# Kernel tuning notes

Hardware: AMD Instinct MI355X
Metric: run time of the kernel (lower is better)

Reference implementation:

```python
import jax, jax.numpy as jnp
import numpy as np

B, N, H, E = 4, 256, 128, 32

def setup_inputs() -> dict:
    key = jax.random.key(0)
    ks = jax.random.split(key, 7)
    s = 0.05
    return {
        "node_h": jax.random.normal(ks[0], (B, N, H), dtype=jnp.float32),
        "dart_h": jax.random.normal(ks[1], (B, N, N, H), dtype=jnp.float32),
        "edge_x": jax.random.normal(ks[2], (B, N, N, E), dtype=jnp.float32),
        "W1": jax.random.normal(ks[3], (3 * H + E, H), dtype=jnp.float32) * s,
        "b1": jnp.zeros((H,), dtype=jnp.float32),
        "W2": jax.random.normal(ks[4], (H, H), dtype=jnp.float32) * s,
        "b2": jnp.zeros((H,), dtype=jnp.float32),
    }

def reference(node_h, dart_h, edge_x, W1, b1, W2, b2):
    # Split first-layer weight by concat blocks [src | dst | dart_h | edge_x]
    W1s, W1d, W1h, W1e = W1[:H], W1[H:2*H], W1[2*H:3*H], W1[3*H:]
    # Equivalent to mlp(cat([src_expand, dst_expand, dart_h, edge_x])) but
    # computes the small [B,N,H] matmuls before broadcasting to [B,N,N,H].
    pre = (jnp.einsum('bih,hk->bik', node_h, W1s)[:, :, None, :]
           + jnp.einsum('bjh,hk->bjk', node_h, W1d)[:, None, :, :]
           + jnp.einsum('bijh,hk->bijk', dart_h, W1h)
           + jnp.einsum('bije,ek->bijk', edge_x, W1e)
           + b1)
    h = jax.nn.relu(pre)
    return jnp.einsum('bijh,hk->bijk', h, W2) + b2
```

## Files before the change

kernel.cpp:

```cpp
#include <hip/hip_runtime.h>
#include <hip/hip_bf16.h>


typedef __attribute__((ext_vector_type(8))) short bf16x8;
typedef __attribute__((ext_vector_type(4))) short bf16x4;
typedef __attribute__((ext_vector_type(4))) float f32x4;

__device__ __forceinline__ unsigned short f2bf(float f) {
  union { float f; unsigned u; } v; v.f = f;
  unsigned r = v.u + 0x7FFFu + ((v.u >> 16) & 1u);
  return (unsigned short)(r >> 16);
}

__global__ void prep_kernel(const float* __restrict__ node, const float* __restrict__ W1,
                            const float* __restrict__ b1, const float* __restrict__ W2,
                            float* __restrict__ S, float* __restrict__ DT,
                            unsigned short* __restrict__ W1hT, unsigned short* __restrict__ W1eT,
                            unsigned short* __restrict__ W2T) {
  const int t = threadIdx.x;
  if (blockIdx.x < 64) {
    __shared__ float nrow[16 * 128];
    const int bi0 = blockIdx.x * 16;
    const float4* src = reinterpret_cast<const float4*>(node + bi0 * 128);
    float4* dst = reinterpret_cast<float4*>(nrow);
    dst[t] = src[t];
    dst[t + 256] = src[t + 256];
    __syncthreads();
    const int kc = t & 127, half = t >> 7;
    float s[8], d[8];
#pragma unroll
    for (int r = 0; r < 8; ++r) { s[r] = 0.f; d[r] = 0.f; }
    for (int h = 0; h < 128; ++h) {
      float ws = W1[h * 128 + kc];
      float wd = W1[(128 + h) * 128 + kc];
#pragma unroll
      for (int r = 0; r < 8; ++r) {
        float nv = nrow[(half * 8 + r) * 128 + h];
        s[r] = fmaf(nv, ws, s[r]);
        d[r] = fmaf(nv, wd, d[r]);
      }
    }
    const float bv = b1[kc];
    const int b = bi0 >> 8, i0 = bi0 & 255;
#pragma unroll
    for (int r = 0; r < 8; ++r) {
      int row = half * 8 + r;
      S[(bi0 + row) * 128 + kc] = s[r] + bv;
      DT[(b * 128 + kc) * 256 + i0 + row] = d[r];
    }
  } else {
    int gid = (blockIdx.x - 64) * 256 + t;
    for (int idx = gid; idx < 16384; idx += 2048)
      W1hT[idx] = f2bf(W1[(256 + (idx & 127)) * 128 + (idx >> 7)]);
    for (int idx = gid; idx < 4096; idx += 2048)
      W1eT[idx] = f2bf(W1[(384 + (idx & 31)) * 128 + (idx >> 5)]);
    for (int idx = gid; idx < 16384; idx += 2048)
      W2T[idx] = f2bf(W2[(idx & 127) * 128 + (idx >> 7)]);
  }
}

#define LDD 136
#define LDE 40

__launch_bounds__(256, 2)
__global__ void fused_kernel(const float* __restrict__ dart, const float* __restrict__ edge,
                             const float* __restrict__ S, const float* __restrict__ DT,
                             const unsigned short* __restrict__ W1hT,
                             const unsigned short* __restrict__ W1eT,
                             const unsigned short* __restrict__ W2T,
                             const float* __restrict__ b2, float* __restrict__ out) {
  __shared__ unsigned short sDart[64 * LDD];
  __shared__ unsigned short sEdge[64 * LDE];
  __shared__ unsigned short sH[64 * LDD];

  const int tid = threadIdx.x;
  const int lane = tid & 63;
  const int w = tid >> 6;
  const int g = lane >> 4;
  const int lj = lane & 15;

  bf16x8 wh[2][4], w2f[4][2], we[2];
#pragma unroll
  for (int kt = 0; kt < 2; ++kt)
#pragma unroll
    for (int hs = 0; hs < 4; ++hs)
      wh[kt][hs] = *reinterpret_cast<const bf16x8*>(&W1hT[(w * 32 + kt * 16 + lj) * 128 + hs * 32 + g * 8]);
#pragma unroll
  for (int kt = 0; kt < 2; ++kt)
    we[kt] = *reinterpret_cast<const bf16x8*>(&W1eT[(w * 32 + kt * 16 + lj) * 32 + g * 8]);
#pragma unroll
  for (int ks = 0; ks < 4; ++ks)
#pragma unroll
    for (int nt = 0; nt < 2; ++nt)
      w2f[ks][nt] = *reinterpret_cast<const bf16x8*>(&W2T[(w * 32 + nt * 16 + lj) * 128 + ks * 32 + g * 8]);
  float b2v[2];
  b2v[0] = b2[w * 32 + lj];
  b2v[1] = b2[w * 32 + 16 + lj];

  for (int tile = blockIdx.x; tile < 4096; tile += gridDim.x) {
    const int m0 = tile * 64;
    const int bi = m0 >> 8;
    const int b = bi >> 8;
    const int j0 = m0 & 255;

    {
      const int row = tid >> 2, c0 = (tid & 3) * 32;
      const float4* src = reinterpret_cast<const float4*>(dart + (size_t)(m0 + row) * 128 + c0);
#pragma unroll
      for (int p = 0; p < 4; ++p) {
        float4 a = src[2 * p], c = src[2 * p + 1];
        bf16x8 pk;
        pk[0] = (short)f2bf(a.x); pk[1] = (short)f2bf(a.y);
        pk[2] = (short)f2bf(a.z); pk[3] = (short)f2bf(a.w);
        pk[4] = (short)f2bf(c.x); pk[5] = (short)f2bf(c.y);
        pk[6] = (short)f2bf(c.z); pk[7] = (short)f2bf(c.w);
        *reinterpret_cast<bf16x8*>(&sDart[row * LDD + c0 + p * 8]) = pk;
      }
      const int e0 = (tid & 3) * 8;
      const float4* esrc = reinterpret_cast<const float4*>(edge + (size_t)(m0 + row) * 32 + e0);
      float4 a = esrc[0], c = esrc[1];
      bf16x8 pk;
      pk[0] = (short)f2bf(a.x); pk[1] = (short)f2bf(a.y);
      pk[2] = (short)f2bf(a.z); pk[3] = (short)f2bf(a.w);
      pk[4] = (short)f2bf(c.x); pk[5] = (short)f2bf(c.y);
      pk[6] = (short)f2bf(c.z); pk[7] = (short)f2bf(c.w);
      *reinterpret_cast<bf16x8*>(&sEdge[row * LDE + e0]) = pk;
    }
    __syncthreads();

    f32x4 acc1[2][4];
#pragma unroll
    for (int kt = 0; kt < 2; ++kt)
#pragma unroll
      for (int jt = 0; jt < 4; ++jt) acc1[kt][jt] = (f32x4){0.f, 0.f, 0.f, 0.f};

#pragma unroll
    for (int hs = 0; hs < 4; ++hs) {
#pragma unroll
      for (int jt = 0; jt < 4; ++jt) {
        bf16x8 bd = *reinterpret_cast<const bf16x8*>(&sDart[(jt * 16 + lj) * LDD + hs * 32 + g * 8]);
        acc1[0][jt] = __builtin_amdgcn_mfma_f32_16x16x32_bf16(wh[0][hs], bd, acc1[0][jt], 0, 0, 0);
        acc1[1][jt] = __builtin_amdgcn_mfma_f32_16x16x32_bf16(wh[1][hs], bd, acc1[1][jt], 0, 0, 0);
      }
    }
#pragma unroll
    for (int jt = 0; jt < 4; ++jt) {
      bf16x8 be = *reinterpret_cast<const bf16x8*>(&sEdge[(jt * 16 + lj) * LDE + g * 8]);
      acc1[0][jt] = __builtin_amdgcn_mfma_f32_16x16x32_bf16(we[0], be, acc1[0][jt], 0, 0, 0);
      acc1[1][jt] = __builtin_amdgcn_mfma_f32_16x16x32_bf16(we[1], be, acc1[1][jt], 0, 0, 0);
    }

    {
      const float* Sp = S + bi * 128 + w * 32;
      const float* DTp = DT + ((b * 128 + w * 32) * 256) + j0;
#pragma unroll
      for (int kt = 0; kt < 2; ++kt) {
        float sv[4];
#pragma unroll
        for (int r = 0; r < 4; ++r) sv[r] = Sp[kt * 16 + g * 4 + r];
#pragma unroll
        for (int jt = 0; jt < 4; ++jt) {
          bf16x4 hp;
#pragma unroll
          for (int r = 0; r < 4; ++r) {
            int kc = kt * 16 + g * 4 + r;
            float dv = DTp[kc * 256 + jt * 16 + lj];
            float x = acc1[kt][jt][r] + sv[r] + dv;
            x = x > 0.f ? x : 0.f;
            hp[r] = (short)f2bf(x);
          }
          *reinterpret_cast<bf16x4*>(&sH[(jt * 16 + lj) * LDD + w * 32 + kt * 16 + g * 4]) = hp;
        }
      }
    }
    __syncthreads();

    f32x4 acc2[4][2];
#pragma unroll
    for (int jt = 0; jt < 4; ++jt)
#pragma unroll
      for (int nt = 0; nt < 2; ++nt) acc2[jt][nt] = (f32x4){0.f, 0.f, 0.f, 0.f};

#pragma unroll
    for (int ks = 0; ks < 4; ++ks) {
#pragma unroll
      for (int jt = 0; jt < 4; ++jt) {
        bf16x8 ah = *reinterpret_cast<const bf16x8*>(&sH[(jt * 16 + lj) * LDD + ks * 32 + g * 8]);
        acc2[jt][0] = __builtin_amdgcn_mfma_f32_16x16x32_bf16(ah, w2f[ks][0], acc2[jt][0], 0, 0, 0);
        acc2[jt][1] = __builtin_amdgcn_mfma_f32_16x16x32_bf16(ah, w2f[ks][1], acc2[jt][1], 0, 0, 0);
      }
    }

    float* op = out + (size_t)m0 * 128 + w * 32;
#pragma unroll
    for (int jt = 0; jt < 4; ++jt)
#pragma unroll
      for (int nt = 0; nt < 2; ++nt)
#pragma unroll
        for (int r = 0; r < 4; ++r)
          op[(size_t)(jt * 16 + g * 4 + r) * 128 + nt * 16 + lj] = acc2[jt][nt][r] + b2v[nt];
  }
}

extern "C" void kernel_launch(void* const* d_in, const int* in_sizes, int n_in,
                              void* d_out, int out_size, void* d_ws, size_t ws_size,
                              hipStream_t stream) {
  const float* node = (const float*)d_in[0];
  const float* dart = (const float*)d_in[1];
  const float* edge = (const float*)d_in[2];
  const float* W1   = (const float*)d_in[3];
  const float* b1   = (const float*)d_in[4];
  const float* W2   = (const float*)d_in[5];
  const float* b2   = (const float*)d_in[6];
  float* out = (float*)d_out;

  float* S  = (float*)d_ws;
  float* DT = S + 131072;
  unsigned short* W1hT = (unsigned short*)(DT + 131072);
  unsigned short* W1eT = W1hT + 16384;
  unsigned short* W2T  = W1eT + 4096;

  hipLaunchKernelGGL(prep_kernel, dim3(72), dim3(256), 0, stream,
                     node, W1, b1, W2, S, DT, W1hT, W1eT, W2T);
  hipLaunchKernelGGL(fused_kernel, dim3(4096), dim3(256), 0, stream,
                     dart, edge, S, DT, W1hT, W1eT, W2T, b2, out);
}
```

Measured before the change: 112.6 us.

## Process one full bi row per block with register prefetch of next tile

Each fused-kernel block now handles one (b,i) row of 256 j across four 64-row tiles. The next tile's dart and edge data are loaded into registers while the current tile's MFMAs run, which overlaps global-load latency with compute, and S and the weights are loaded once per block. The second GEMM swaps its operands so the output can be written as float4 rows, and the prep kernel uses more, smaller blocks for the S/DT precompute. In exchange the grid has fewer blocks and register pressure rises from the prefetch buffers.

```diff
diff --git a/kernel.cpp b/kernel.cpp
--- a/kernel.cpp
+++ b/kernel.cpp
@@ -18,38 +18,30 @@
                             unsigned short* __restrict__ W1hT, unsigned short* __restrict__ W1eT,
                             unsigned short* __restrict__ W2T) {
   const int t = threadIdx.x;
-  if (blockIdx.x < 64) {
-    __shared__ float nrow[16 * 128];
-    const int bi0 = blockIdx.x * 16;
-    const float4* src = reinterpret_cast<const float4*>(node + bi0 * 128);
-    float4* dst = reinterpret_cast<float4*>(nrow);
-    dst[t] = src[t];
-    dst[t + 256] = src[t + 256];
+  if (blockIdx.x < 256) {
+    __shared__ float nrow[4 * 128];
+    const int bi0 = blockIdx.x * 4;
+    if (t < 128)
+      reinterpret_cast<float4*>(nrow)[t] = reinterpret_cast<const float4*>(node + bi0 * 128)[t];
     __syncthreads();
     const int kc = t & 127, half = t >> 7;
-    float s[8], d[8];
-#pragma unroll
-    for (int r = 0; r < 8; ++r) { s[r] = 0.f; d[r] = 0.f; }
+    float s0 = 0.f, s1 = 0.f, d0 = 0.f, d1 = 0.f;
     for (int h = 0; h < 128; ++h) {
       float ws = W1[h * 128 + kc];
       float wd = W1[(128 + h) * 128 + kc];
-#pragma unroll
-      for (int r = 0; r < 8; ++r) {
-        float nv = nrow[(half * 8 + r) * 128 + h];
-        s[r] = fmaf(nv, ws, s[r]);
-        d[r] = fmaf(nv, wd, d[r]);
-      }
+      float n0 = nrow[(half * 2) * 128 + h];
+      float n1 = nrow[(half * 2 + 1) * 128 + h];
+      s0 = fmaf(n0, ws, s0); s1 = fmaf(n1, ws, s1);
+      d0 = fmaf(n0, wd, d0); d1 = fmaf(n1, wd, d1);
     }
     const float bv = b1[kc];
     const int b = bi0 >> 8, i0 = bi0 & 255;
-#pragma unroll
-    for (int r = 0; r < 8; ++r) {
-      int row = half * 8 + r;
-      S[(bi0 + row) * 128 + kc] = s[r] + bv;
-      DT[(b * 128 + kc) * 256 + i0 + row] = d[r];
-    }
+    S[(bi0 + half * 2) * 128 + kc] = s0 + bv;
+    S[(bi0 + half * 2 + 1) * 128 + kc] = s1 + bv;
+    DT[(b * 128 + kc) * 256 + i0 + half * 2] = d0;
+    DT[(b * 128 + kc) * 256 + i0 + half * 2 + 1] = d1;
   } else {
-    int gid = (blockIdx.x - 64) * 256 + t;
+    int gid = (blockIdx.x - 256) * 256 + t;
     for (int idx = gid; idx < 16384; idx += 2048)
       W1hT[idx] = f2bf(W1[(256 + (idx & 127)) * 128 + (idx >> 7)]);
     for (int idx = gid; idx < 4096; idx += 2048)
@@ -79,6 +71,10 @@
   const int g = lane >> 4;
   const int lj = lane & 15;
 
+  const int bi = blockIdx.x;
+  const int b = bi >> 8;
+  const size_t m_base = (size_t)bi * 256;
+
   bf16x8 wh[2][4], w2f[4][2], we[2];
 #pragma unroll
   for (int kt = 0; kt < 2; ++kt)
@@ -93,112 +89,165 @@
 #pragma unroll
     for (int nt = 0; nt < 2; ++nt)
       w2f[ks][nt] = *reinterpret_cast<const bf16x8*>(&W2T[(w * 32 + nt * 16 + lj) * 128 + ks * 32 + g * 8]);
-  float b2v[2];
-  b2v[0] = b2[w * 32 + lj];
-  b2v[1] = b2[w * 32 + 16 + lj];
-
-  for (int tile = blockIdx.x; tile < 4096; tile += gridDim.x) {
-    const int m0 = tile * 64;
-    const int bi = m0 >> 8;
-    const int b = bi >> 8;
-    const int j0 = m0 & 255;
-
+
+  float sv[2][4], b2v[2][4];
+#pragma unroll
+  for (int kt = 0; kt < 2; ++kt)
+#pragma unroll
+    for (int r = 0; r < 4; ++r)
+      sv[kt][r] = S[bi * 128 + w * 32 + kt * 16 + g * 4 + r];
+#pragma unroll
+  for (int nt = 0; nt < 2; ++nt)
+#pragma unroll
+    for (int r = 0; r < 4; ++r)
+      b2v[nt][r] = b2[w * 32 + nt * 16 + g * 4 + r];
+
+  const int srow = tid >> 2;
+  const int c0 = (tid & 3) * 32;
+  const int e0 = (tid & 3) * 8;
+
+  float4 rD[8], rE[2];
+
+  {
+    const float4* dsrc = reinterpret_cast<const float4*>(dart + (m_base + srow) * 128 + c0);
+#pragma unroll
+    for (int p = 0; p < 8; ++p) rD[p] = dsrc[p];
+    const float4* esrc = reinterpret_cast<const float4*>(edge + (m_base + srow) * 32 + e0);
+    rE[0] = esrc[0]; rE[1] = esrc[1];
+  }
+  {
+#pragma unroll
+    for (int p = 0; p < 4; ++p) {
+      float4 a = rD[2 * p], c = rD[2 * p + 1];
+      bf16x8 pk;
+      pk[0] = (short)f2bf(a.x); pk[1] = (short)f2bf(a.y);
+      pk[2] = (short)f2bf(a.z); pk[3] = (short)f2bf(a.w);
+      pk[4] = (short)f2bf(c.x); pk[5] = (short)f2bf(c.y);
+      pk[6] = (short)f2bf(c.z); pk[7] = (short)f2bf(c.w);
+      *reinterpret_cast<bf16x8*>(&sDart[srow * LDD + c0 + p * 8]) = pk;
+    }
+    float4 a = rE[0], c = rE[1];
+    bf16x8 pk;
+    pk[0] = (short)f2bf(a.x); pk[1] = (short)f2bf(a.y);
+    pk[2] = (short)f2bf(a.z); pk[3] = (short)f2bf(a.w);
+    pk[4] = (short)f2bf(c.x); pk[5] = (short)f2bf(c.y);
+    pk[6] = (short)f2bf(c.z); pk[7] = (short)f2bf(c.w);
+    *reinterpret_cast<bf16x8*>(&sEdge[srow * LDE + e0]) = pk;
+  }
+  __syncthreads();
+
+  for (int t = 0; t < 4; ++t) {
+    const int j0 = t * 64;
+
+    float dv[2][4][4];
     {
-      const int row = tid >> 2, c0 = (tid & 3) * 32;
-      const float4* src = reinterpret_cast<const float4*>(dart + (size_t)(m0 + row) * 128 + c0);
+      const float* DTp = DT + (size_t)(b * 128 + w * 32) * 256 + j0;
+#pragma unroll
+      for (int kt = 0; kt < 2; ++kt)
+#pragma unroll
+        for (int jt = 0; jt < 4; ++jt)
+#pragma unroll
+          for (int r = 0; r < 4; ++r)
+            dv[kt][jt][r] = DTp[(kt * 16 + g * 4 + r) * 256 + jt * 16 + lj];
+    }
+
+    if (t < 3) {
+      const float4* dsrc = reinterpret_cast<const float4*>(dart + (m_base + j0 + 64 + srow) * 128 + c0);
+#pragma unroll
+      for (int p = 0; p < 8; ++p) rD[p] = dsrc[p];
+      const float4* esrc = reinterpret_cast<const float4*>(edge + (m_base + j0 + 64 + srow) * 32 + e0);
+      rE[0] = esrc[0]; rE[1] = esrc[1];
+    }
+
+    f32x4 acc1[2][4];
+#pragma unroll
+    for (int kt = 0; kt < 2; ++kt)
+#pragma unroll
+      for (int jt = 0; jt < 4; ++jt) acc1[kt][jt] = (f32x4){0.f, 0.f, 0.f, 0.f};
+
+#pragma unroll
+    for (int hs = 0; hs < 4; ++hs) {
+#pragma unroll
+      for (int jt = 0; jt < 4; ++jt) {
+        bf16x8 bd = *reinterpret_cast<const bf16x8*>(&sDart[(jt * 16 + lj) * LDD + hs * 32 + g * 8]);
+        acc1[0][jt] = __builtin_amdgcn_mfma_f32_16x16x32_bf16(wh[0][hs], bd, acc1[0][jt], 0, 0, 0);
+        acc1[1][jt] = __builtin_amdgcn_mfma_f32_16x16x32_bf16(wh[1][hs], bd, acc1[1][jt], 0, 0, 0);
+      }
+    }
+#pragma unroll
+    for (int jt = 0; jt < 4; ++jt) {
+      bf16x8 be = *reinterpret_cast<const bf16x8*>(&sEdge[(jt * 16 + lj) * LDE + e0 - (tid & 3) * 8 + g * 8]);
+      acc1[0][jt] = __builtin_amdgcn_mfma_f32_16x16x32_bf16(we[0], be, acc1[0][jt], 0, 0, 0);
+      acc1[1][jt] = __builtin_amdgcn_mfma_f32_16x16x32_bf16(we[1], be, acc1[1][jt], 0, 0, 0);
+    }
+
+#pragma unroll
+    for (int kt = 0; kt < 2; ++kt) {
+#pragma unroll
+      for (int jt = 0; jt < 4; ++jt) {
+        bf16x4 hp;
+#pragma unroll
+        for (int r = 0; r < 4; ++r) {
+          float x = acc1[kt][jt][r] + sv[kt][r] + dv[kt][jt][r];
+          x = x > 0.f ? x : 0.f;
+          hp[r] = (short)f2bf(x);
+        }
+        *reinterpret_cast<bf16x4*>(&sH[(jt * 16 + lj) * LDD + w * 32 + kt * 16 + g * 4]) = hp;
+      }
+    }
+    __syncthreads();
+
+    f32x4 acc2[4][2];
+#pragma unroll
+    for (int jt = 0; jt < 4; ++jt)
+#pragma unroll
+      for (int nt = 0; nt < 2; ++nt) acc2[jt][nt] = (f32x4){0.f, 0.f, 0.f, 0.f};
+
+#pragma unroll
+    for (int ks = 0; ks < 4; ++ks) {
+#pragma unroll
+      for (int jt = 0; jt < 4; ++jt) {
+        bf16x8 ah = *reinterpret_cast<const bf16x8*>(&sH[(jt * 16 + lj) * LDD + ks * 32 + g * 8]);
+        acc2[jt][0] = __builtin_amdgcn_mfma_f32_16x16x32_bf16(w2f[ks][0], ah, acc2[jt][0], 0, 0, 0);
+        acc2[jt][1] = __builtin_amdgcn_mfma_f32_16x16x32_bf16(w2f[ks][1], ah, acc2[jt][1], 0, 0, 0);
+      }
+    }
+
+    if (t < 3) {
 #pragma unroll
       for (int p = 0; p < 4; ++p) {
-        float4 a = src[2 * p], c = src[2 * p + 1];
+        float4 a = rD[2 * p], c = rD[2 * p + 1];
         bf16x8 pk;
         pk[0] = (short)f2bf(a.x); pk[1] = (short)f2bf(a.y);
         pk[2] = (short)f2bf(a.z); pk[3] = (short)f2bf(a.w);
         pk[4] = (short)f2bf(c.x); pk[5] = (short)f2bf(c.y);
         pk[6] = (short)f2bf(c.z); pk[7] = (short)f2bf(c.w);
-        *reinterpret_cast<bf16x8*>(&sDart[row * LDD + c0 + p * 8]) = pk;
-      }
-      const int e0 = (tid & 3) * 8;
-      const float4* esrc = reinterpret_cast<const float4*>(edge + (size_t)(m0 + row) * 32 + e0);
-      float4 a = esrc[0], c = esrc[1];
+        *reinterpret_cast<bf16x8*>(&sDart[srow * LDD + c0 + p * 8]) = pk;
+      }
+      float4 a = rE[0], c = rE[1];
       bf16x8 pk;
       pk[0] = (short)f2bf(a.x); pk[1] = (short)f2bf(a.y);
       pk[2] = (short)f2bf(a.z); pk[3] = (short)f2bf(a.w);
       pk[4] = (short)f2bf(c.x); pk[5] = (short)f2bf(c.y);
       pk[6] = (short)f2bf(c.z); pk[7] = (short)f2bf(c.w);
-      *reinterpret_cast<bf16x8*>(&sEdge[row * LDE + e0]) = pk;
+      *reinterpret_cast<bf16x8*>(&sEdge[srow * LDE + e0]) = pk;
+    }
+
+    {
+      float* op = out + (m_base + j0) * 128;
+#pragma unroll
+      for (int jt = 0; jt < 4; ++jt)
+#pragma unroll
+        for (int nt = 0; nt < 2; ++nt) {
+          float4 v;
+          v.x = acc2[jt][nt][0] + b2v[nt][0];
+          v.y = acc2[jt][nt][1] + b2v[nt][1];
+          v.z = acc2[jt][nt][2] + b2v[nt][2];
+          v.w = acc2[jt][nt][3] + b2v[nt][3];
+          *reinterpret_cast<float4*>(&op[(size_t)(jt * 16 + lj) * 128 + w * 32 + nt * 16 + g * 4]) = v;
+        }
     }
     __syncthreads();
-
-    f32x4 acc1[2][4];
-#pragma unroll
-    for (int kt = 0; kt < 2; ++kt)
-#pragma unroll
-      for (int jt = 0; jt < 4; ++jt) acc1[kt][jt] = (f32x4){0.f, 0.f, 0.f, 0.f};
-
-#pragma unroll
-    for (int hs = 0; hs < 4; ++hs) {
-#pragma unroll
-      for (int jt = 0; jt < 4; ++jt) {
-        bf16x8 bd = *reinterpret_cast<const bf16x8*>(&sDart[(jt * 16 + lj) * LDD + hs * 32 + g * 8]);
-        acc1[0][jt] = __builtin_amdgcn_mfma_f32_16x16x32_bf16(wh[0][hs], bd, acc1[0][jt], 0, 0, 0);
-        acc1[1][jt] = __builtin_amdgcn_mfma_f32_16x16x32_bf16(wh[1][hs], bd, acc1[1][jt], 0, 0, 0);
-      }
-    }
-#pragma unroll
-    for (int jt = 0; jt < 4; ++jt) {
-      bf16x8 be = *reinterpret_cast<const bf16x8*>(&sEdge[(jt * 16 + lj) * LDE + g * 8]);
-      acc1[0][jt] = __builtin_amdgcn_mfma_f32_16x16x32_bf16(we[0], be, acc1[0][jt], 0, 0, 0);
-      acc1[1][jt] = __builtin_amdgcn_mfma_f32_16x16x32_bf16(we[1], be, acc1[1][jt], 0, 0, 0);
-    }
-
-    {
-      const float* Sp = S + bi * 128 + w * 32;
-      const float* DTp = DT + ((b * 128 + w * 32) * 256) + j0;
-#pragma unroll
-      for (int kt = 0; kt < 2; ++kt) {
-        float sv[4];
-#pragma unroll
-        for (int r = 0; r < 4; ++r) sv[r] = Sp[kt * 16 + g * 4 + r];
-#pragma unroll
-        for (int jt = 0; jt < 4; ++jt) {
-          bf16x4 hp;
-#pragma unroll
-          for (int r = 0; r < 4; ++r) {
-            int kc = kt * 16 + g * 4 + r;
-            float dv = DTp[kc * 256 + jt * 16 + lj];
-            float x = acc1[kt][jt][r] + sv[r] + dv;
-            x = x > 0.f ? x : 0.f;
-            hp[r] = (short)f2bf(x);
-          }
-          *reinterpret_cast<bf16x4*>(&sH[(jt * 16 + lj) * LDD + w * 32 + kt * 16 + g * 4]) = hp;
-        }
-      }
-    }
-    __syncthreads();
-
-    f32x4 acc2[4][2];
-#pragma unroll
-    for (int jt = 0; jt < 4; ++jt)
-#pragma unroll
-      for (int nt = 0; nt < 2; ++nt) acc2[jt][nt] = (f32x4){0.f, 0.f, 0.f, 0.f};
-
-#pragma unroll
-    for (int ks = 0; ks < 4; ++ks) {
-#pragma unroll
-      for (int jt = 0; jt < 4; ++jt) {
-        bf16x8 ah = *reinterpret_cast<const bf16x8*>(&sH[(jt * 16 + lj) * LDD + ks * 32 + g * 8]);
-        acc2[jt][0] = __builtin_amdgcn_mfma_f32_16x16x32_bf16(ah, w2f[ks][0], acc2[jt][0], 0, 0, 0);
-        acc2[jt][1] = __builtin_amdgcn_mfma_f32_16x16x32_bf16(ah, w2f[ks][1], acc2[jt][1], 0, 0, 0);
-      }
-    }
-
-    float* op = out + (size_t)m0 * 128 + w * 32;
-#pragma unroll
-    for (int jt = 0; jt < 4; ++jt)
-#pragma unroll
-      for (int nt = 0; nt < 2; ++nt)
-#pragma unroll
-        for (int r = 0; r < 4; ++r)
-          op[(size_t)(jt * 16 + g * 4 + r) * 128 + nt * 16 + lj] = acc2[jt][nt][r] + b2v[nt];
   }
 }
 
@@ -220,8 +269,8 @@
   unsigned short* W1eT = W1hT + 16384;
   unsigned short* W2T  = W1eT + 4096;
 
-  hipLaunchKernelGGL(prep_kernel, dim3(72), dim3(256), 0, stream,
+  hipLaunchKernelGGL(prep_kernel, dim3(264), dim3(256), 0, stream,
                      node, W1, b1, W2, S, DT, W1hT, W1eT, W2T);
-  hipLaunchKernelGGL(fused_kernel, dim3(4096), dim3(256), 0, stream,
+  hipLaunchKernelGGL(fused_kernel, dim3(1024), dim3(256), 0, stream,
                      dart, edge, S, DT, W1hT, W1eT, W2T, b2, out);
 }
```

After: 93.81 us. -16.7%, faster.
